# Kernel tuning notes

Hardware: AMD Instinct MI355X
Metric: run time of the kernel (lower is better)

Reference implementation:

```python
import jax, jax.numpy as jnp
import numpy as np
from jax import lax

B, N, R, L = 16, 256, 24, 32
MEAN_STOP_TIME_S = 60.0
AVG_TRANSFER_WAIT_TIME_S = 300.0
SYMMETRIC_ROUTES = True
INF = jnp.inf


def setup_inputs() -> dict:
    key = jax.random.key(0)
    k1, k2, k3 = jax.random.split(key, 3)
    drive_times = jax.random.uniform(k1, (B, N, N), jnp.float32) * 1000.0 + 30.0
    demand = jax.random.uniform(k2, (B, N, N), jnp.float32) * 10.0
    demand = demand * (1.0 - jnp.eye(N, dtype=jnp.float32))  # no self-demand
    batch_routes = jax.random.randint(k3, (B, R, L), 0, N, dtype=jnp.int32)
    return {"drive_times": drive_times, "demand": demand, "batch_routes": batch_routes}


def _route_edges_and_legs(routes, dtm):
    # routes: [B,R,L] node ids (no -1 padding in this setup); dtm: [B,N,N]
    b = jnp.arange(B)[:, None, None]
    sf, st = routes[:, :, :-1], routes[:, :, 1:]
    leg_fwd = dtm[b, sf, st] + MEAN_STOP_TIME_S            # [B,R,L-1]
    zero = jnp.zeros((B, R, 1), dtm.dtype)
    cum_f = jnp.concatenate([zero, jnp.cumsum(leg_fwd, -1)], -1)  # [B,R,L]
    tri = jnp.triu(jnp.ones((L, L), dtype=bool), 1)
    # ride time from stop position i to position j>i along the route
    t_f = jnp.where(tri, cum_f[:, :, None, :] - cum_f[:, :, :, None], INF)
    b4 = jnp.arange(B)[:, None, None, None]
    src = jnp.broadcast_to(routes[:, :, :, None], (B, R, L, L))
    dst = jnp.broadcast_to(routes[:, :, None, :], (B, R, L, L))
    edge = jnp.full((B, N, N), INF, dtm.dtype)
    edge = edge.at[b4, src, dst].min(t_f)
    leg_rev = None
    if SYMMETRIC_ROUTES:
        leg_rev = dtm[b, st, sf] + MEAN_STOP_TIME_S        # reverse-direction legs
        cum_r = jnp.concatenate([zero, jnp.cumsum(leg_rev, -1)], -1)
        t_r = jnp.where(tri, cum_r[:, :, None, :] - cum_r[:, :, :, None], INF)
        edge = edge.at[b4, dst, src].min(t_r)              # ride from s_j back to s_i
    return edge, leg_fwd, leg_rev


def _floyd_warshall(edge):
    # batched FW, also tracking hop count of shortest paths
    idx = jnp.arange(N)
    dist = edge.at[:, idx, idx].set(0.0)
    offdiag = ~jnp.eye(N, dtype=bool)
    hops = jnp.where(jnp.isfinite(dist) & offdiag, 1.0, 0.0)

    def body(carry, k):
        d, h = carry
        dc = lax.dynamic_slice_in_dim(d, k, 1, axis=2)  # [B,N,1]
        dr = lax.dynamic_slice_in_dim(d, k, 1, axis=1)  # [B,1,N]
        hc = lax.dynamic_slice_in_dim(h, k, 1, axis=2)
        hr = lax.dynamic_slice_in_dim(h, k, 1, axis=1)
        alt = dc + dr
        better = alt < d
        return (jnp.where(better, alt, d), jnp.where(better, hc + hr, h)), None

    (dist, hops), _ = lax.scan(body, (dist, hops), idx)
    return dist, hops


def reference(drive_times, demand, batch_routes):
    edge, leg_fwd, leg_rev = _route_edges_and_legs(batch_routes, drive_times)
    dist, hops = _floyd_warshall(edge)
    nopath = jnp.isinf(dist)
    path_lens = jnp.where(nopath, 0.0, hops + 1.0)  # n nodes on path (diag -> 1)
    transfers = jnp.where(path_lens == 0.0, 0.0, path_lens - 2.0)
    trip_times = jnp.where(nopath, 0.0, dist + transfers * AVG_TRANSFER_WAIT_TIME_S)
    total_demand_time = (demand * trip_times).sum((1, 2))
    total_transfers = (demand * transfers).sum((1, 2))
    unserved_demand = jnp.where(nopath, demand, 0.0).sum((1, 2))
    total_demand = demand.sum((1, 2))
    n_disconnected = (nopath & (demand > 0)).sum((1, 2))
    buckets = [jnp.where(transfers == float(ii), demand, 0.0).sum((1, 2)) for ii in range(3)]
    d_un = jnp.where(transfers > 2.0, demand, 0.0).sum((1, 2)) + unserved_demand
    trips_at_transfers = jnp.stack(buckets + [d_un], axis=1)  # [B,4]
    total_route_time = leg_fwd.sum((1, 2))
    if SYMMETRIC_ROUTES:
        total_route_time = total_route_time + leg_rev.sum((1, 2))
    return (total_demand_time, total_route_time, trips_at_transfers,
            total_demand, unserved_demand, total_transfers, trip_times,
            n_disconnected)
```

## Files before the change

### kernel.cpp

```cpp
#include <hip/hip_runtime.h>

#define BB 16
#define NL 256
#define RR 24
#define LL 32
#define NN (NL*NL)
#define BNN (BB*NN)
#define TT 64

#define O_TDT 0
#define O_RT  16
#define O_TAT 32
#define O_TD  96
#define O_UNS 112
#define O_TTR 128
#define O_TT  144
#define O_ND  1048720

#define HSC 9.3132257461547852e-10
#define H2  1073741824.0
#define HMASK 8191

#define RIDX(r, c2) (((r)<<6) + ((((c2) ^ ((r)&31)))<<1))
#define LDD(A, r, c2) (*(double2*)&A[RIDX((r),(c2))])

__global__ __launch_bounds__(1024) void k_init(double2* __restrict__ dist2, float* __restrict__ acc){
    int idx = blockIdx.x*1024 + threadIdx.x;
    double inf = __builtin_huge_val();
    double2 v = make_double2(inf, inf);
    int q = (idx*2) & (NN-1);
    int r = q % 257;
    if (r == 0)   v.x = 0.0;
    if (r == 256) v.y = 0.0;
    dist2[idx] = v;
    if (blockIdx.x == 0 && threadIdx.x < 256) acc[threadIdx.x] = 0.f;
}

__global__ void k_routes(const float* __restrict__ dtm, const int* __restrict__ routes,
                         unsigned long long* __restrict__ dist, float* __restrict__ acc){
    int br = blockIdx.x; int b = br / RR, r = br % RR;
    int lane = threadIdx.x;
    __shared__ int   s[LL];
    __shared__ float lf[LL], lr[LL], cf[LL], cr[LL];
    if (lane < LL) s[lane] = routes[(b*RR + r)*LL + lane];
    __syncthreads();
    if (lane < LL-1){
        int a0 = s[lane], a1 = s[lane+1];
        const float* dt = dtm + b*NN;
        lf[lane] = dt[a0*NL + a1] + 60.0f;
        lr[lane] = dt[a1*NL + a0] + 60.0f;
    }
    __syncthreads();
    if (lane == 0){
        float af = 0.f, ar = 0.f;
        cf[0] = 0.f; cr[0] = 0.f;
        for (int l = 0; l < LL-1; l++){
            af += lf[l]; ar += lr[l];
            cf[l+1] = af; cr[l+1] = ar;
        }
        atomicAdd(&acc[b*16 + 1], af + ar);
    }
    __syncthreads();
    for (int p = lane; p < LL*LL; p += 64){
        int i = p >> 5, j = p & 31;
        if (j > i){
            double vf = (double)(cf[j] - cf[i]) + HSC;
            double vr = (double)(cr[j] - cr[i]) + HSC;
            atomicMin(&dist[b*NN + s[i]*NL + s[j]], (unsigned long long)__double_as_longlong(vf));
            atomicMin(&dist[b*NN + s[j]*NL + s[i]], (unsigned long long)__double_as_longlong(vr));
        }
    }
}

__global__ __launch_bounds__(256, 1) void k_fw_round(
        const double* __restrict__ src, double* __restrict__ dst, int kb){
    int b  = blockIdx.y;
    int m  = blockIdx.x;
    int ti = m >> 2, tj = m & 3;
    int t  = threadIdx.x;
    int r0 = (t >> 4) << 2;
    int c2 = (t & 15) << 1;
    int c4 = (t & 15) << 2;
    __shared__ double KD[4096];
    __shared__ double BD[4096];
    const double* Kg = src + b*NN + kb*TT*(NL+1);
    const double* Bg = src + b*NN + kb*TT*NL + tj*TT;
    const double* Cg = src + b*NN + ti*TT*NL + kb*TT;
    const double* Dg = src + b*NN + ti*TT*NL + tj*TT;

    double2 c0[4][2], d0[4][2];
    #pragma unroll
    for (int i = 0; i < 4; i++){
        c0[i][0] = *(const double2*)(Cg + (r0+i)*NL + c4);
        c0[i][1] = *(const double2*)(Cg + (r0+i)*NL + c4 + 2);
        d0[i][0] = *(const double2*)(Dg + (r0+i)*NL + c4);
        d0[i][1] = *(const double2*)(Dg + (r0+i)*NL + c4 + 2);
    }

    #pragma unroll
    for (int u = 0; u < 8; u++){
        int fid = u*256 + t;
        int row = fid >> 5, cc = fid & 31;
        LDD(KD, row, cc) = *(const double2*)(Kg + row*NL + cc*2);
        LDD(BD, row, cc) = *(const double2*)(Bg + row*NL + cc*2);
    }
    __syncthreads();

    for (int skb = 0; skb < 4; skb++){
        int s0 = skb*16, sc2 = skb*8;
        if (t < 64){
            int i = t >> 2, jg = t & 3, rr = s0 + i, cb = sc2 + jg*2;
            double2 m0 = LDD(KD, rr, cb), m1 = LDD(KD, rr, cb+1);
            double md4[4] = {m0.x, m0.y, m1.x, m1.y};
            #pragma unroll
            for (int k = 0; k < 16; k++){
                double rd[4];
                #pragma unroll
                for (int c = 0; c < 4; c++) rd[c] = __shfl(md4[c], (k<<2)|jg);
                double cd = __shfl(md4[k&3], (i<<2)|(k>>2));
                #pragma unroll
                for (int c = 0; c < 4; c++) md4[c] = fmin(md4[c], cd + rd[c]);
            }
            LDD(KD, rr, cb)   = make_double2(md4[0], md4[1]);
            LDD(KD, rr, cb+1) = make_double2(md4[2], md4[3]);
        }
        __syncthreads();
        int rs_r  = s0 + (t >> 4);
        int rs_c2 = (t & 15) << 1;
        int cs_r  = t >> 2;
        int cs_c2 = sc2 + ((t & 3) << 1);
        double rs[4], cs[4], ar[16], ac[16];
        {
            double2 v0 = LDD(KD, rs_r, rs_c2), v1 = LDD(KD, rs_r, rs_c2+1);
            rs[0]=v0.x; rs[1]=v0.y; rs[2]=v1.x; rs[3]=v1.y;
            double2 w0 = LDD(KD, cs_r, cs_c2), w1 = LDD(KD, cs_r, cs_c2+1);
            cs[0]=w0.x; cs[1]=w0.y; cs[2]=w1.x; cs[3]=w1.y;
            #pragma unroll
            for (int c = 0; c < 8; c++){
                double2 av = LDD(KD, rs_r, sc2 + c);
                ar[2*c] = av.x; ar[2*c+1] = av.y;
                double2 aw = LDD(KD, cs_r, sc2 + c);
                ac[2*c] = aw.x; ac[2*c+1] = aw.y;
            }
        }
        #pragma unroll
        for (int k = 0; k < 16; k++){
            double2 b0 = LDD(KD, s0+k, rs_c2), b1 = LDD(KD, s0+k, rs_c2+1);
            rs[0] = fmin(rs[0], ar[k] + b0.x);
            rs[1] = fmin(rs[1], ar[k] + b0.y);
            rs[2] = fmin(rs[2], ar[k] + b1.x);
            rs[3] = fmin(rs[3], ar[k] + b1.y);
            double2 e0 = LDD(KD, s0+k, cs_c2), e1 = LDD(KD, s0+k, cs_c2+1);
            cs[0] = fmin(cs[0], ac[k] + e0.x);
            cs[1] = fmin(cs[1], ac[k] + e0.y);
            cs[2] = fmin(cs[2], ac[k] + e1.x);
            cs[3] = fmin(cs[3], ac[k] + e1.y);
        }
        __syncthreads();
        LDD(KD, rs_r, rs_c2)   = make_double2(rs[0], rs[1]);
        LDD(KD, rs_r, rs_c2+1) = make_double2(rs[2], rs[3]);
        LDD(KD, cs_r, cs_c2)   = make_double2(cs[0], cs[1]);
        LDD(KD, cs_r, cs_c2+1) = make_double2(cs[2], cs[3]);
        __syncthreads();
        double dd[4][4];
        #pragma unroll
        for (int i = 0; i < 4; i++){
            double2 v0 = LDD(KD, r0+i, c2), v1 = LDD(KD, r0+i, c2+1);
            dd[i][0]=v0.x; dd[i][1]=v0.y; dd[i][2]=v1.x; dd[i][3]=v1.y;
        }
        #pragma unroll
        for (int q4 = 0; q4 < 4; q4++){
            int kr = s0 + q4*4;
            double a[4][4], bm[4][4];
            #pragma unroll
            for (int i = 0; i < 4; i++){
                double2 a0 = LDD(KD, r0+i, sc2+q4*2), a1 = LDD(KD, r0+i, sc2+q4*2+1);
                a[i][0]=a0.x; a[i][1]=a0.y; a[i][2]=a1.x; a[i][3]=a1.y;
            }
            #pragma unroll
            for (int q = 0; q < 4; q++){
                double2 b0 = LDD(KD, kr+q, c2), b1 = LDD(KD, kr+q, c2+1);
                bm[q][0]=b0.x; bm[q][1]=b0.y; bm[q][2]=b1.x; bm[q][3]=b1.y;
            }
            #pragma unroll
            for (int q = 0; q < 4; q++)
            #pragma unroll
            for (int i = 0; i < 4; i++)
            #pragma unroll
            for (int j = 0; j < 4; j++)
                dd[i][j] = fmin(dd[i][j], a[i][q] + bm[q][j]);
        }
        __syncthreads();
        #pragma unroll
        for (int i = 0; i < 4; i++){
            LDD(KD, r0+i, c2)   = make_double2(dd[i][0], dd[i][1]);
            LDD(KD, r0+i, c2+1) = make_double2(dd[i][2], dd[i][3]);
        }
        __syncthreads();
    }

    double inf = __builtin_huge_val();
    double md[4][4];
    #pragma unroll
    for (int i = 0; i < 4; i++)
    #pragma unroll
    for (int j = 0; j < 4; j++) md[i][j] = inf;
    #pragma unroll 4
    for (int q4 = 0; q4 < 16; q4++){
        double a[4][4], bm[4][4];
        #pragma unroll
        for (int i = 0; i < 4; i++){
            double2 a0 = LDD(KD, r0+i, q4*2), a1 = LDD(KD, r0+i, q4*2+1);
            a[i][0]=a0.x; a[i][1]=a0.y; a[i][2]=a1.x; a[i][3]=a1.y;
        }
        int kr = q4*4;
        #pragma unroll
        for (int q = 0; q < 4; q++){
            double2 b0 = LDD(BD, kr+q, c2), b1 = LDD(BD, kr+q, c2+1);
            bm[q][0]=b0.x; bm[q][1]=b0.y; bm[q][2]=b1.x; bm[q][3]=b1.y;
        }
        #pragma unroll
        for (int q = 0; q < 4; q++)
        #pragma unroll
        for (int i = 0; i < 4; i++)
        #pragma unroll
        for (int j = 0; j < 4; j++)
            md[i][j] = fmin(md[i][j], a[i][q] + bm[q][j]);
    }
    __syncthreads();
    #pragma unroll
    for (int i = 0; i < 4; i++){
        LDD(BD, r0+i, c2)   = make_double2(md[i][0], md[i][1]);
        LDD(BD, r0+i, c2+1) = make_double2(md[i][2], md[i][3]);
        LDD(KD, r0+i, c2)   = c0[i][0];
        LDD(KD, r0+i, c2+1) = c0[i][1];
    }
    __syncthreads();

    double dd[4][4];
    #pragma unroll
    for (int i = 0; i < 4; i++){
        dd[i][0]=d0[i][0].x; dd[i][1]=d0[i][0].y; dd[i][2]=d0[i][1].x; dd[i][3]=d0[i][1].y;
    }
    #pragma unroll 4
    for (int q4 = 0; q4 < 16; q4++){
        double a[4][4], bm[4][4];
        #pragma unroll
        for (int i = 0; i < 4; i++){
            double2 a0 = LDD(KD, r0+i, q4*2), a1 = LDD(KD, r0+i, q4*2+1);
            a[i][0]=a0.x; a[i][1]=a0.y; a[i][2]=a1.x; a[i][3]=a1.y;
        }
        int kr = q4*4;
        #pragma unroll
        for (int q = 0; q < 4; q++){
            double2 b0 = LDD(BD, kr+q, c2), b1 = LDD(BD, kr+q, c2+1);
            bm[q][0]=b0.x; bm[q][1]=b0.y; bm[q][2]=b1.x; bm[q][3]=b1.y;
        }
        #pragma unroll
        for (int q = 0; q < 4; q++)
        #pragma unroll
        for (int i = 0; i < 4; i++)
        #pragma unroll
        for (int j = 0; j < 4; j++)
            dd[i][j] = fmin(dd[i][j], a[i][q] + bm[q][j]);
    }
    double* Od = dst + b*NN + ti*TT*NL + tj*TT;
    #pragma unroll
    for (int i = 0; i < 4; i++){
        *(double2*)(Od + (r0+i)*NL + c4)     = make_double2(dd[i][0], dd[i][1]);
        *(double2*)(Od + (r0+i)*NL + c4 + 2) = make_double2(dd[i][2], dd[i][3]);
    }
}

__global__ __launch_bounds__(1024) void k_epi(const double2* __restrict__ dist2,
        const float4* __restrict__ demand4, float* __restrict__ out, float* __restrict__ acc){
    int b = blockIdx.y;
    int fid = (b*NN >> 2) + blockIdx.x*1024 + threadIdx.x;
    long long q2 = (long long)fid * 2;
    double2 va = dist2[q2], vb = dist2[q2+1];
    double vs[4] = {va.x, va.y, vb.x, vb.y};
    float4 mv = demand4[fid];
    float ms[4] = {mv.x, mv.y, mv.z, mv.w};
    float s0=0,s1=0,s2=0,s3=0,s4=0,s5=0,s6=0,s7=0,s8=0;
    float tts[4];
    #pragma unroll
    for (int e = 0; e < 4; e++){
        double v = vs[e];
        bool np = !(v < 1e37);
        double vv = np ? 0.0 : v;
        int h = (int)(((long long)(vv * H2)) & (long long)HMASK);
        float d = (float)vv;
        float dm = ms[e];
        float pl = np ? 0.f : (float)(h + 1);
        float tr = (pl == 0.f) ? 0.f : pl - 2.f;
        float tt = np ? 0.f : d + tr*300.f;
        tts[e] = tt;
        s0 += dm*tt;
        s1 += dm*tr;
        s2 += np ? dm : 0.f;
        s3 += dm;
        s4 += (np && dm > 0.f) ? 1.f : 0.f;
        s5 += (tr == 0.f) ? dm : 0.f;
        s6 += (tr == 1.f) ? dm : 0.f;
        s7 += (tr == 2.f) ? dm : 0.f;
        s8 += (tr > 2.f) ? dm : 0.f;
    }
    ((float4*)(out + O_TT))[fid] = make_float4(tts[0],tts[1],tts[2],tts[3]);
    #define RED(x) { x += __shfl_down(x,32); x += __shfl_down(x,16); x += __shfl_down(x,8); \
                     x += __shfl_down(x,4);  x += __shfl_down(x,2);  x += __shfl_down(x,1); }
    RED(s0) RED(s1) RED(s2) RED(s3) RED(s4) RED(s5) RED(s6) RED(s7) RED(s8)
    __shared__ float red[16][9];
    int w = threadIdx.x >> 6;
    if ((threadIdx.x & 63) == 0){
        red[w][0]=s0; red[w][1]=s1; red[w][2]=s2; red[w][3]=s3; red[w][4]=s4;
        red[w][5]=s5; red[w][6]=s6; red[w][7]=s7; red[w][8]=s8;
    }
    __syncthreads();
    if (threadIdx.x < 9){
        float v = 0.f;
        #pragma unroll
        for (int ww = 0; ww < 16; ww++) v += red[ww][threadIdx.x];
        int slot = (threadIdx.x == 0) ? 0 : threadIdx.x + 1;
        atomicAdd(&acc[b*16 + slot], v);
    }
    __syncthreads();
    __shared__ int isLast;
    if (threadIdx.x == 0){
        unsigned prev = atomicAdd((unsigned int*)(acc + 255), 1u);
        isLast = (prev == 255u) ? 1 : 0;
    }
    __syncthreads();
    if (isLast && threadIdx.x < BB){
        int bb = threadIdx.x;
        float a[10];
        #pragma unroll
        for (int s = 0; s < 10; s++) a[s] = atomicAdd(&acc[bb*16 + s], 0.f);
        out[O_TDT + bb] = a[0];
        out[O_RT  + bb] = a[1];
        out[O_TAT + 4*bb + 0] = a[6];
        out[O_TAT + 4*bb + 1] = a[7];
        out[O_TAT + 4*bb + 2] = a[8];
        out[O_TAT + 4*bb + 3] = a[9] + a[3];
        out[O_TD  + bb] = a[4];
        out[O_UNS + bb] = a[3];
        out[O_TTR + bb] = a[2];
        out[O_ND  + bb] = a[5];
    }
}

extern "C" void kernel_launch(void* const* d_in, const int* in_sizes, int n_in,
                              void* d_out, int out_size, void* d_ws, size_t ws_size,
                              hipStream_t stream){
    (void)in_sizes; (void)n_in; (void)out_size; (void)ws_size;
    const float* dtm    = (const float*)d_in[0];
    const float* demand = (const float*)d_in[1];
    const int*   routes = (const int*)d_in[2];
    float* out   = (float*)d_out;
    double* distA = (double*)d_ws;
    double* distB = distA + BNN;
    float*  acc   = (float*)(distB + BNN);

    k_init  <<<512, 1024, 0, stream>>>((double2*)distA, acc);
    k_routes<<<BB*RR,  64, 0, stream>>>(dtm, routes, (unsigned long long*)distA, acc);
    k_fw_round<<<dim3(16,BB), 256, 0, stream>>>(distA, distB, 0);
    k_fw_round<<<dim3(16,BB), 256, 0, stream>>>(distB, distA, 1);
    k_fw_round<<<dim3(16,BB), 256, 0, stream>>>(distA, distB, 2);
    k_fw_round<<<dim3(16,BB), 256, 0, stream>>>(distB, distA, 3);
    k_epi<<<dim3(16,BB), 1024, 0, stream>>>((const double2*)distA,
                                            (const float4*)demand, out, acc);
}
```

Baseline: 256.5 us.

## Fuse init, routes, blocked FW rounds and epilogue into one persistent kernel

Replaces the seven kernel launches with a single persistent kernel of 256 blocks, one per tile per batch, that synchronises the blocks of each batch through per-batch global atomic barriers. Each block keeps its tile in registers across the Floyd-Warshall rounds and writes it back to global memory only when other tiles need it. The epilogue reduction runs directly from registers, so the final distance matrix is never re-read from memory. This removes launch gaps and global round trips, but depends on all 256 blocks being resident at once to avoid a deadlock, and adds spin-wait barrier cost.

```diff
diff --git a/kernel.cpp b/kernel.cpp
--- a/kernel.cpp
+++ b/kernel.cpp
@@ -24,327 +24,359 @@
 #define RIDX(r, c2) (((r)<<6) + ((((c2) ^ ((r)&31)))<<1))
 #define LDD(A, r, c2) (*(double2*)&A[RIDX((r),(c2))])
 
-__global__ __launch_bounds__(1024) void k_init(double2* __restrict__ dist2, float* __restrict__ acc){
-    int idx = blockIdx.x*1024 + threadIdx.x;
-    double inf = __builtin_huge_val();
-    double2 v = make_double2(inf, inf);
-    int q = (idx*2) & (NN-1);
-    int r = q % 257;
-    if (r == 0)   v.x = 0.0;
-    if (r == 256) v.y = 0.0;
-    dist2[idx] = v;
-    if (blockIdx.x == 0 && threadIdx.x < 256) acc[threadIdx.x] = 0.f;
-}
-
-__global__ void k_routes(const float* __restrict__ dtm, const int* __restrict__ routes,
-                         unsigned long long* __restrict__ dist, float* __restrict__ acc){
-    int br = blockIdx.x; int b = br / RR, r = br % RR;
-    int lane = threadIdx.x;
-    __shared__ int   s[LL];
-    __shared__ float lf[LL], lr[LL], cf[LL], cr[LL];
-    if (lane < LL) s[lane] = routes[(b*RR + r)*LL + lane];
+__global__ __launch_bounds__(512) void k_init0(unsigned* __restrict__ ctr){
+    ctr[threadIdx.x] = 0u;
+}
+
+static __device__ __forceinline__ void bbar(unsigned* c, unsigned tgt){
     __syncthreads();
-    if (lane < LL-1){
-        int a0 = s[lane], a1 = s[lane+1];
-        const float* dt = dtm + b*NN;
-        lf[lane] = dt[a0*NL + a1] + 60.0f;
-        lr[lane] = dt[a1*NL + a0] + 60.0f;
+    if (threadIdx.x == 0){
+        __hip_atomic_fetch_add(c, 1u, __ATOMIC_RELEASE, __HIP_MEMORY_SCOPE_AGENT);
+        while (__hip_atomic_load(c, __ATOMIC_ACQUIRE, __HIP_MEMORY_SCOPE_AGENT) < tgt)
+            __builtin_amdgcn_s_sleep(2);
     }
     __syncthreads();
-    if (lane == 0){
-        float af = 0.f, ar = 0.f;
-        cf[0] = 0.f; cr[0] = 0.f;
-        for (int l = 0; l < LL-1; l++){
-            af += lf[l]; ar += lr[l];
-            cf[l+1] = af; cr[l+1] = ar;
-        }
-        atomicAdd(&acc[b*16 + 1], af + ar);
-    }
-    __syncthreads();
-    for (int p = lane; p < LL*LL; p += 64){
-        int i = p >> 5, j = p & 31;
-        if (j > i){
-            double vf = (double)(cf[j] - cf[i]) + HSC;
-            double vr = (double)(cr[j] - cr[i]) + HSC;
-            atomicMin(&dist[b*NN + s[i]*NL + s[j]], (unsigned long long)__double_as_longlong(vf));
-            atomicMin(&dist[b*NN + s[j]*NL + s[i]], (unsigned long long)__double_as_longlong(vr));
-        }
-    }
-}
-
-__global__ __launch_bounds__(256, 1) void k_fw_round(
-        const double* __restrict__ src, double* __restrict__ dst, int kb){
-    int b  = blockIdx.y;
-    int m  = blockIdx.x;
+}
+
+static __device__ __forceinline__ void mulAcc(double dd[4][4], double* A, double* Bm,
+                                              int r0, int cA, int cB){
+    #pragma unroll 4
+    for (int q4 = 0; q4 < 16; q4++){
+        int kr = q4*4, kc = q4*2;
+        double a[4][4], bm[4][4];
+        #pragma unroll
+        for (int i = 0; i < 4; i++){
+            double2 a0 = LDD(A, r0+i, kc), a1 = LDD(A, r0+i, kc+1);
+            a[i][0]=a0.x; a[i][1]=a0.y; a[i][2]=a1.x; a[i][3]=a1.y;
+        }
+        #pragma unroll
+        for (int q = 0; q < 4; q++){
+            double2 b0 = LDD(Bm, kr+q, cA), b1 = LDD(Bm, kr+q, cB);
+            bm[q][0]=b0.x; bm[q][1]=b0.y; bm[q][2]=b1.x; bm[q][3]=b1.y;
+        }
+        #pragma unroll
+        for (int q = 0; q < 4; q++)
+        #pragma unroll
+        for (int i = 0; i < 4; i++)
+        #pragma unroll
+        for (int j = 0; j < 4; j++)
+            dd[i][j] = fmin(dd[i][j], a[i][q] + bm[q][j]);
+    }
+}
+
+static __device__ __forceinline__ void close64(double* SA, int t, int r0, int cA, int cB){
+    for (int skb = 0; skb < 4; skb++){
+        int s0 = skb*16, sc2 = skb*8;
+        if (t < 64){
+            int i = t >> 2, jg = t & 3, rr = s0 + i, cbk = sc2 + jg*2;
+            double2 m0 = LDD(SA, rr, cbk), m1 = LDD(SA, rr, cbk+1);
+            double md4[4] = {m0.x, m0.y, m1.x, m1.y};
+            #pragma unroll
+            for (int k = 0; k < 16; k++){
+                double rd[4];
+                #pragma unroll
+                for (int c = 0; c < 4; c++) rd[c] = __shfl(md4[c], (k<<2)|jg);
+                double cd = __shfl(md4[k&3], (i<<2)|(k>>2));
+                #pragma unroll
+                for (int c = 0; c < 4; c++) md4[c] = fmin(md4[c], cd + rd[c]);
+            }
+            LDD(SA, rr, cbk)   = make_double2(md4[0], md4[1]);
+            LDD(SA, rr, cbk+1) = make_double2(md4[2], md4[3]);
+        }
+        __syncthreads();
+        double sv[2][4], av[2][16];
+        int wr, wcA, wcB;
+        if (t < 128){
+            wr  = s0 + ((t >> 4) << 1);
+            wcA = t & 15; wcB = wcA + 16;
+        } else {
+            int t2 = t - 128;
+            wr  = (t2 >> 2) << 1;
+            wcA = sc2 + (t2 & 3); wcB = wcA + 4;
+        }
+        #pragma unroll
+        for (int i = 0; i < 2; i++){
+            double2 v0 = LDD(SA, wr+i, wcA), v1 = LDD(SA, wr+i, wcB);
+            sv[i][0]=v0.x; sv[i][1]=v0.y; sv[i][2]=v1.x; sv[i][3]=v1.y;
+            #pragma unroll
+            for (int c = 0; c < 8; c++){
+                double2 av2 = LDD(SA, wr+i, sc2 + c);
+                av[i][2*c] = av2.x; av[i][2*c+1] = av2.y;
+            }
+        }
+        #pragma unroll
+        for (int k = 0; k < 16; k++){
+            double2 b0 = LDD(SA, s0+k, wcA), b1 = LDD(SA, s0+k, wcB);
+            #pragma unroll
+            for (int i = 0; i < 2; i++){
+                double ak = av[i][k];
+                sv[i][0] = fmin(sv[i][0], ak + b0.x);
+                sv[i][1] = fmin(sv[i][1], ak + b0.y);
+                sv[i][2] = fmin(sv[i][2], ak + b1.x);
+                sv[i][3] = fmin(sv[i][3], ak + b1.y);
+            }
+        }
+        __syncthreads();
+        #pragma unroll
+        for (int i = 0; i < 2; i++){
+            LDD(SA, wr+i, wcA) = make_double2(sv[i][0], sv[i][1]);
+            LDD(SA, wr+i, wcB) = make_double2(sv[i][2], sv[i][3]);
+        }
+        __syncthreads();
+        double e[4][4];
+        #pragma unroll
+        for (int i = 0; i < 4; i++){
+            double2 v0 = LDD(SA, r0+i, cA), v1 = LDD(SA, r0+i, cB);
+            e[i][0]=v0.x; e[i][1]=v0.y; e[i][2]=v1.x; e[i][3]=v1.y;
+        }
+        #pragma unroll
+        for (int q4 = 0; q4 < 4; q4++){
+            int kr = s0 + q4*4, kc = sc2 + q4*2;
+            double a[4][4], bm[4][4];
+            #pragma unroll
+            for (int i = 0; i < 4; i++){
+                double2 a0 = LDD(SA, r0+i, kc), a1 = LDD(SA, r0+i, kc+1);
+                a[i][0]=a0.x; a[i][1]=a0.y; a[i][2]=a1.x; a[i][3]=a1.y;
+            }
+            #pragma unroll
+            for (int q = 0; q < 4; q++){
+                double2 b0 = LDD(SA, kr+q, cA), b1 = LDD(SA, kr+q, cB);
+                bm[q][0]=b0.x; bm[q][1]=b0.y; bm[q][2]=b1.x; bm[q][3]=b1.y;
+            }
+            #pragma unroll
+            for (int q = 0; q < 4; q++)
+            #pragma unroll
+            for (int i = 0; i < 4; i++)
+            #pragma unroll
+            for (int j = 0; j < 4; j++)
+                e[i][j] = fmin(e[i][j], a[i][q] + bm[q][j]);
+        }
+        __syncthreads();
+        #pragma unroll
+        for (int i = 0; i < 4; i++){
+            LDD(SA, r0+i, cA) = make_double2(e[i][0], e[i][1]);
+            LDD(SA, r0+i, cB) = make_double2(e[i][2], e[i][3]);
+        }
+        __syncthreads();
+    }
+}
+
+__global__ __launch_bounds__(256, 1) void k_mega(
+        const float* __restrict__ dtm, const int* __restrict__ routes,
+        const float* __restrict__ demand, double* __restrict__ D,
+        float* __restrict__ out, float* __restrict__ acc, unsigned* __restrict__ ctr){
+    int blk = blockIdx.x;
+    int b = blk >> 4, m = blk & 15;
     int ti = m >> 2, tj = m & 3;
     int t  = threadIdx.x;
     int r0 = (t >> 4) << 2;
-    int c2 = (t & 15) << 1;
-    int c4 = (t & 15) << 2;
-    __shared__ double KD[4096];
-    __shared__ double BD[4096];
-    const double* Kg = src + b*NN + kb*TT*(NL+1);
-    const double* Bg = src + b*NN + kb*TT*NL + tj*TT;
-    const double* Cg = src + b*NN + ti*TT*NL + kb*TT;
-    const double* Dg = src + b*NN + ti*TT*NL + tj*TT;
-
-    double2 c0[4][2], d0[4][2];
+    int cA = t & 15, cB = cA + 16;
+    unsigned* cbp = ctr + b*32;
+    double* Tg = D + b*NN + (ti*NL + tj)*TT;
+    __shared__ __align__(16) double SA[4096], SB[4096];
+
+    double inf = __builtin_huge_val();
     #pragma unroll
     for (int i = 0; i < 4; i++){
-        c0[i][0] = *(const double2*)(Cg + (r0+i)*NL + c4);
-        c0[i][1] = *(const double2*)(Cg + (r0+i)*NL + c4 + 2);
-        d0[i][0] = *(const double2*)(Dg + (r0+i)*NL + c4);
-        d0[i][1] = *(const double2*)(Dg + (r0+i)*NL + c4 + 2);
-    }
-
-    #pragma unroll
-    for (int u = 0; u < 8; u++){
-        int fid = u*256 + t;
-        int row = fid >> 5, cc = fid & 31;
-        LDD(KD, row, cc) = *(const double2*)(Kg + row*NL + cc*2);
-        LDD(BD, row, cc) = *(const double2*)(Bg + row*NL + cc*2);
-    }
-    __syncthreads();
-
-    for (int skb = 0; skb < 4; skb++){
-        int s0 = skb*16, sc2 = skb*8;
-        if (t < 64){
-            int i = t >> 2, jg = t & 3, rr = s0 + i, cb = sc2 + jg*2;
-            double2 m0 = LDD(KD, rr, cb), m1 = LDD(KD, rr, cb+1);
-            double md4[4] = {m0.x, m0.y, m1.x, m1.y};
-            #pragma unroll
-            for (int k = 0; k < 16; k++){
-                double rd[4];
-                #pragma unroll
-                for (int c = 0; c < 4; c++) rd[c] = __shfl(md4[c], (k<<2)|jg);
-                double cd = __shfl(md4[k&3], (i<<2)|(k>>2));
-                #pragma unroll
-                for (int c = 0; c < 4; c++) md4[c] = fmin(md4[c], cd + rd[c]);
-            }
-            LDD(KD, rr, cb)   = make_double2(md4[0], md4[1]);
-            LDD(KD, rr, cb+1) = make_double2(md4[2], md4[3]);
-        }
-        __syncthreads();
-        int rs_r  = s0 + (t >> 4);
-        int rs_c2 = (t & 15) << 1;
-        int cs_r  = t >> 2;
-        int cs_c2 = sc2 + ((t & 3) << 1);
-        double rs[4], cs[4], ar[16], ac[16];
-        {
-            double2 v0 = LDD(KD, rs_r, rs_c2), v1 = LDD(KD, rs_r, rs_c2+1);
-            rs[0]=v0.x; rs[1]=v0.y; rs[2]=v1.x; rs[3]=v1.y;
-            double2 w0 = LDD(KD, cs_r, cs_c2), w1 = LDD(KD, cs_r, cs_c2+1);
-            cs[0]=w0.x; cs[1]=w0.y; cs[2]=w1.x; cs[3]=w1.y;
-            #pragma unroll
-            for (int c = 0; c < 8; c++){
-                double2 av = LDD(KD, rs_r, sc2 + c);
-                ar[2*c] = av.x; ar[2*c+1] = av.y;
-                double2 aw = LDD(KD, cs_r, sc2 + c);
-                ac[2*c] = aw.x; ac[2*c+1] = aw.y;
-            }
-        }
-        #pragma unroll
-        for (int k = 0; k < 16; k++){
-            double2 b0 = LDD(KD, s0+k, rs_c2), b1 = LDD(KD, s0+k, rs_c2+1);
-            rs[0] = fmin(rs[0], ar[k] + b0.x);
-            rs[1] = fmin(rs[1], ar[k] + b0.y);
-            rs[2] = fmin(rs[2], ar[k] + b1.x);
-            rs[3] = fmin(rs[3], ar[k] + b1.y);
-            double2 e0 = LDD(KD, s0+k, cs_c2), e1 = LDD(KD, s0+k, cs_c2+1);
-            cs[0] = fmin(cs[0], ac[k] + e0.x);
-            cs[1] = fmin(cs[1], ac[k] + e0.y);
-            cs[2] = fmin(cs[2], ac[k] + e1.x);
-            cs[3] = fmin(cs[3], ac[k] + e1.y);
-        }
-        __syncthreads();
-        LDD(KD, rs_r, rs_c2)   = make_double2(rs[0], rs[1]);
-        LDD(KD, rs_r, rs_c2+1) = make_double2(rs[2], rs[3]);
-        LDD(KD, cs_r, cs_c2)   = make_double2(cs[0], cs[1]);
-        LDD(KD, cs_r, cs_c2+1) = make_double2(cs[2], cs[3]);
-        __syncthreads();
-        double dd[4][4];
-        #pragma unroll
-        for (int i = 0; i < 4; i++){
-            double2 v0 = LDD(KD, r0+i, c2), v1 = LDD(KD, r0+i, c2+1);
-            dd[i][0]=v0.x; dd[i][1]=v0.y; dd[i][2]=v1.x; dd[i][3]=v1.y;
-        }
-        #pragma unroll
-        for (int q4 = 0; q4 < 4; q4++){
-            int kr = s0 + q4*4;
-            double a[4][4], bm[4][4];
+        double2 z0 = make_double2(inf, inf), z1 = z0;
+        if (ti == tj){
+            int gr = r0 + i;
+            if (gr == 2*cA)   z0.x = 0.0;
+            if (gr == 2*cA+1) z0.y = 0.0;
+            if (gr == 2*cB)   z1.x = 0.0;
+            if (gr == 2*cB+1) z1.y = 0.0;
+        }
+        *(double2*)(Tg + (r0+i)*NL + 2*cA) = z0;
+        *(double2*)(Tg + (r0+i)*NL + 2*cB) = z1;
+    }
+    if (m == 0 && t < 16) acc[b*16 + t] = 0.f;
+    bbar(cbp, 16u*1);
+
+    {
+        int w = t >> 6, lane = t & 63;
+        int r = (w == 0) ? m : ((w == 1 && m < 8) ? 16 + m : -1);
+        char* rbase = (char*)SA + w*1024;
+        int*   sS = (int*)rbase;
+        float* lf = (float*)(rbase + 128);
+        float* lr = (float*)(rbase + 256);
+        float* cf = (float*)(rbase + 384);
+        float* cr = (float*)(rbase + 512);
+        if (r >= 0 && lane < LL) sS[lane] = routes[(b*RR + r)*LL + lane];
+        __syncthreads();
+        if (r >= 0 && lane < LL-1){
+            int a0 = sS[lane], a1 = sS[lane+1];
+            const float* dt = dtm + b*NN;
+            lf[lane] = dt[a0*NL + a1] + 60.0f;
+            lr[lane] = dt[a1*NL + a0] + 60.0f;
+        }
+        __syncthreads();
+        if (r >= 0 && lane == 0){
+            float af = 0.f, ar2 = 0.f;
+            cf[0] = 0.f; cr[0] = 0.f;
+            for (int l = 0; l < LL-1; l++){
+                af += lf[l]; ar2 += lr[l];
+                cf[l+1] = af; cr[l+1] = ar2;
+            }
+            atomicAdd(&acc[b*16 + 1], af + ar2);
+        }
+        __syncthreads();
+        if (r >= 0){
+            unsigned long long* db = (unsigned long long*)(D + b*NN);
+            for (int p = lane; p < LL*LL; p += 64){
+                int i = p >> 5, j = p & 31;
+                if (j > i){
+                    double vf = (double)(cf[j] - cf[i]) + HSC;
+                    double vr = (double)(cr[j] - cr[i]) + HSC;
+                    atomicMin(&db[sS[i]*NL + sS[j]], (unsigned long long)__double_as_longlong(vf));
+                    atomicMin(&db[sS[j]*NL + sS[i]], (unsigned long long)__double_as_longlong(vr));
+                }
+            }
+        }
+    }
+    bbar(cbp, 16u*2);
+
+    double dd[4][4];
+    #pragma unroll
+    for (int i = 0; i < 4; i++){
+        double2 v0 = *(const double2*)(Tg + (r0+i)*NL + 2*cA);
+        double2 v1 = *(const double2*)(Tg + (r0+i)*NL + 2*cB);
+        dd[i][0]=v0.x; dd[i][1]=v0.y; dd[i][2]=v1.x; dd[i][3]=v1.y;
+    }
+
+    for (int kb = 0; kb < 4; kb++){
+        bool isDiag = (ti == kb) & (tj == kb);
+        bool isRow  = (ti == kb) && !isDiag;
+        bool isCol  = (tj == kb) && !isDiag;
+        bool inDP   = isDiag | isRow | isCol;
+        if (inDP){
+            if (isDiag){
+                #pragma unroll
+                for (int i = 0; i < 4; i++){
+                    LDD(SA, r0+i, cA) = make_double2(dd[i][0], dd[i][1]);
+                    LDD(SA, r0+i, cB) = make_double2(dd[i][2], dd[i][3]);
+                }
+            } else {
+                #pragma unroll
+                for (int i = 0; i < 4; i++){
+                    LDD(SB, r0+i, cA) = make_double2(dd[i][0], dd[i][1]);
+                    LDD(SB, r0+i, cB) = make_double2(dd[i][2], dd[i][3]);
+                }
+                const double* Kg = D + b*NN + kb*TT*(NL+1);
+                #pragma unroll
+                for (int u = 0; u < 8; u++){
+                    int fid = u*256 + t, row = fid >> 5, cc = fid & 31;
+                    LDD(SA, row, cc) = *(const double2*)(Kg + row*NL + cc*2);
+                }
+            }
+            __syncthreads();
+            close64(SA, t, r0, cA, cB);
+            if (isDiag){
+                #pragma unroll
+                for (int i = 0; i < 4; i++){
+                    double2 v0 = LDD(SA, r0+i, cA), v1 = LDD(SA, r0+i, cB);
+                    dd[i][0]=v0.x; dd[i][1]=v0.y; dd[i][2]=v1.x; dd[i][3]=v1.y;
+                }
+            } else if (isRow){
+                mulAcc(dd, SA, SB, r0, cA, cB);
+            } else {
+                mulAcc(dd, SB, SA, r0, cA, cB);
+            }
             #pragma unroll
             for (int i = 0; i < 4; i++){
-                double2 a0 = LDD(KD, r0+i, sc2+q4*2), a1 = LDD(KD, r0+i, sc2+q4*2+1);
-                a[i][0]=a0.x; a[i][1]=a0.y; a[i][2]=a1.x; a[i][3]=a1.y;
-            }
-            #pragma unroll
-            for (int q = 0; q < 4; q++){
-                double2 b0 = LDD(KD, kr+q, c2), b1 = LDD(KD, kr+q, c2+1);
-                bm[q][0]=b0.x; bm[q][1]=b0.y; bm[q][2]=b1.x; bm[q][3]=b1.y;
-            }
-            #pragma unroll
-            for (int q = 0; q < 4; q++)
-            #pragma unroll
-            for (int i = 0; i < 4; i++)
-            #pragma unroll
-            for (int j = 0; j < 4; j++)
-                dd[i][j] = fmin(dd[i][j], a[i][q] + bm[q][j]);
-        }
-        __syncthreads();
-        #pragma unroll
-        for (int i = 0; i < 4; i++){
-            LDD(KD, r0+i, c2)   = make_double2(dd[i][0], dd[i][1]);
-            LDD(KD, r0+i, c2+1) = make_double2(dd[i][2], dd[i][3]);
-        }
-        __syncthreads();
-    }
-
-    double inf = __builtin_huge_val();
-    double md[4][4];
-    #pragma unroll
-    for (int i = 0; i < 4; i++)
-    #pragma unroll
-    for (int j = 0; j < 4; j++) md[i][j] = inf;
-    #pragma unroll 4
-    for (int q4 = 0; q4 < 16; q4++){
-        double a[4][4], bm[4][4];
-        #pragma unroll
-        for (int i = 0; i < 4; i++){
-            double2 a0 = LDD(KD, r0+i, q4*2), a1 = LDD(KD, r0+i, q4*2+1);
-            a[i][0]=a0.x; a[i][1]=a0.y; a[i][2]=a1.x; a[i][3]=a1.y;
-        }
-        int kr = q4*4;
-        #pragma unroll
-        for (int q = 0; q < 4; q++){
-            double2 b0 = LDD(BD, kr+q, c2), b1 = LDD(BD, kr+q, c2+1);
-            bm[q][0]=b0.x; bm[q][1]=b0.y; bm[q][2]=b1.x; bm[q][3]=b1.y;
-        }
-        #pragma unroll
-        for (int q = 0; q < 4; q++)
-        #pragma unroll
-        for (int i = 0; i < 4; i++)
-        #pragma unroll
-        for (int j = 0; j < 4; j++)
-            md[i][j] = fmin(md[i][j], a[i][q] + bm[q][j]);
-    }
-    __syncthreads();
+                *(double2*)(Tg + (r0+i)*NL + 2*cA) = make_double2(dd[i][0], dd[i][1]);
+                *(double2*)(Tg + (r0+i)*NL + 2*cB) = make_double2(dd[i][2], dd[i][3]);
+            }
+        }
+        bbar(cbp, 16u*(3 + 2*kb));
+        if (!inDP){
+            const double* Xg = D + b*NN + (ti*NL + kb)*TT;
+            const double* Yg = D + b*NN + (kb*NL + tj)*TT;
+            #pragma unroll
+            for (int u = 0; u < 8; u++){
+                int fid = u*256 + t, row = fid >> 5, cc = fid & 31;
+                LDD(SA, row, cc) = *(const double2*)(Xg + row*NL + cc*2);
+                LDD(SB, row, cc) = *(const double2*)(Yg + row*NL + cc*2);
+            }
+            __syncthreads();
+            mulAcc(dd, SA, SB, r0, cA, cB);
+            if (kb != 3){
+                #pragma unroll
+                for (int i = 0; i < 4; i++){
+                    *(double2*)(Tg + (r0+i)*NL + 2*cA) = make_double2(dd[i][0], dd[i][1]);
+                    *(double2*)(Tg + (r0+i)*NL + 2*cB) = make_double2(dd[i][2], dd[i][3]);
+                }
+            }
+        }
+        bbar(cbp, 16u*(4 + 2*kb));
+    }
+
+    float s9[9];
+    #pragma unroll
+    for (int q = 0; q < 9; q++) s9[q] = 0.f;
     #pragma unroll
     for (int i = 0; i < 4; i++){
-        LDD(BD, r0+i, c2)   = make_double2(md[i][0], md[i][1]);
-        LDD(BD, r0+i, c2+1) = make_double2(md[i][2], md[i][3]);
-        LDD(KD, r0+i, c2)   = c0[i][0];
-        LDD(KD, r0+i, c2+1) = c0[i][1];
-    }
-    __syncthreads();
-
-    double dd[4][4];
-    #pragma unroll
-    for (int i = 0; i < 4; i++){
-        dd[i][0]=d0[i][0].x; dd[i][1]=d0[i][0].y; dd[i][2]=d0[i][1].x; dd[i][3]=d0[i][1].y;
-    }
-    #pragma unroll 4
-    for (int q4 = 0; q4 < 16; q4++){
-        double a[4][4], bm[4][4];
-        #pragma unroll
-        for (int i = 0; i < 4; i++){
-            double2 a0 = LDD(KD, r0+i, q4*2), a1 = LDD(KD, r0+i, q4*2+1);
-            a[i][0]=a0.x; a[i][1]=a0.y; a[i][2]=a1.x; a[i][3]=a1.y;
-        }
-        int kr = q4*4;
-        #pragma unroll
-        for (int q = 0; q < 4; q++){
-            double2 b0 = LDD(BD, kr+q, c2), b1 = LDD(BD, kr+q, c2+1);
-            bm[q][0]=b0.x; bm[q][1]=b0.y; bm[q][2]=b1.x; bm[q][3]=b1.y;
-        }
-        #pragma unroll
-        for (int q = 0; q < 4; q++)
-        #pragma unroll
-        for (int i = 0; i < 4; i++)
-        #pragma unroll
-        for (int j = 0; j < 4; j++)
-            dd[i][j] = fmin(dd[i][j], a[i][q] + bm[q][j]);
-    }
-    double* Od = dst + b*NN + ti*TT*NL + tj*TT;
-    #pragma unroll
-    for (int i = 0; i < 4; i++){
-        *(double2*)(Od + (r0+i)*NL + c4)     = make_double2(dd[i][0], dd[i][1]);
-        *(double2*)(Od + (r0+i)*NL + c4 + 2) = make_double2(dd[i][2], dd[i][3]);
-    }
-}
-
-__global__ __launch_bounds__(1024) void k_epi(const double2* __restrict__ dist2,
-        const float4* __restrict__ demand4, float* __restrict__ out, float* __restrict__ acc){
-    int b = blockIdx.y;
-    int fid = (b*NN >> 2) + blockIdx.x*1024 + threadIdx.x;
-    long long q2 = (long long)fid * 2;
-    double2 va = dist2[q2], vb = dist2[q2+1];
-    double vs[4] = {va.x, va.y, vb.x, vb.y};
-    float4 mv = demand4[fid];
-    float ms[4] = {mv.x, mv.y, mv.z, mv.w};
-    float s0=0,s1=0,s2=0,s3=0,s4=0,s5=0,s6=0,s7=0,s8=0;
-    float tts[4];
-    #pragma unroll
-    for (int e = 0; e < 4; e++){
-        double v = vs[e];
-        bool np = !(v < 1e37);
-        double vv = np ? 0.0 : v;
-        int h = (int)(((long long)(vv * H2)) & (long long)HMASK);
-        float d = (float)vv;
-        float dm = ms[e];
-        float pl = np ? 0.f : (float)(h + 1);
-        float tr = (pl == 0.f) ? 0.f : pl - 2.f;
-        float tt = np ? 0.f : d + tr*300.f;
-        tts[e] = tt;
-        s0 += dm*tt;
-        s1 += dm*tr;
-        s2 += np ? dm : 0.f;
-        s3 += dm;
-        s4 += (np && dm > 0.f) ? 1.f : 0.f;
-        s5 += (tr == 0.f) ? dm : 0.f;
-        s6 += (tr == 1.f) ? dm : 0.f;
-        s7 += (tr == 2.f) ? dm : 0.f;
-        s8 += (tr > 2.f) ? dm : 0.f;
-    }
-    ((float4*)(out + O_TT))[fid] = make_float4(tts[0],tts[1],tts[2],tts[3]);
+        const float* dmg = demand + b*NN + (ti*TT + r0 + i)*NL + tj*TT;
+        float* ttg = out + O_TT + b*NN + (ti*TT + r0 + i)*NL + tj*TT;
+        float2 m0 = *(const float2*)(dmg + 2*cA);
+        float2 m1 = *(const float2*)(dmg + 2*cB);
+        float dmv[4] = {m0.x, m0.y, m1.x, m1.y};
+        float tts[4];
+        #pragma unroll
+        for (int e = 0; e < 4; e++){
+            double v = dd[i][e];
+            bool np = !(v < 1e37);
+            double vv = np ? 0.0 : v;
+            int h = (int)(((long long)(vv * H2)) & (long long)HMASK);
+            float d = (float)vv;
+            float dm = dmv[e];
+            float pl = np ? 0.f : (float)(h + 1);
+            float tr = (pl == 0.f) ? 0.f : pl - 2.f;
+            float tt = np ? 0.f : d + tr*300.f;
+            tts[e] = tt;
+            s9[0] += dm*tt;
+            s9[1] += dm*tr;
+            s9[2] += np ? dm : 0.f;
+            s9[3] += dm;
+            s9[4] += (np && dm > 0.f) ? 1.f : 0.f;
+            s9[5] += (tr == 0.f) ? dm : 0.f;
+            s9[6] += (tr == 1.f) ? dm : 0.f;
+            s9[7] += (tr == 2.f) ? dm : 0.f;
+            s9[8] += (tr > 2.f) ? dm : 0.f;
+        }
+        *(float2*)(ttg + 2*cA) = make_float2(tts[0], tts[1]);
+        *(float2*)(ttg + 2*cB) = make_float2(tts[2], tts[3]);
+    }
     #define RED(x) { x += __shfl_down(x,32); x += __shfl_down(x,16); x += __shfl_down(x,8); \
                      x += __shfl_down(x,4);  x += __shfl_down(x,2);  x += __shfl_down(x,1); }
-    RED(s0) RED(s1) RED(s2) RED(s3) RED(s4) RED(s5) RED(s6) RED(s7) RED(s8)
-    __shared__ float red[16][9];
-    int w = threadIdx.x >> 6;
-    if ((threadIdx.x & 63) == 0){
-        red[w][0]=s0; red[w][1]=s1; red[w][2]=s2; red[w][3]=s3; red[w][4]=s4;
-        red[w][5]=s5; red[w][6]=s6; red[w][7]=s7; red[w][8]=s8;
+    #pragma unroll
+    for (int q = 0; q < 9; q++) RED(s9[q])
+    float* red = (float*)SB;
+    int wv = t >> 6;
+    if ((t & 63) == 0){
+        #pragma unroll
+        for (int q = 0; q < 9; q++) red[wv*9 + q] = s9[q];
     }
     __syncthreads();
-    if (threadIdx.x < 9){
-        float v = 0.f;
-        #pragma unroll
-        for (int ww = 0; ww < 16; ww++) v += red[ww][threadIdx.x];
-        int slot = (threadIdx.x == 0) ? 0 : threadIdx.x + 1;
+    if (t < 9){
+        float v = red[t] + red[9+t] + red[18+t] + red[27+t];
+        int slot = (t == 0) ? 0 : t + 1;
         atomicAdd(&acc[b*16 + slot], v);
     }
-    __syncthreads();
-    __shared__ int isLast;
-    if (threadIdx.x == 0){
-        unsigned prev = atomicAdd((unsigned int*)(acc + 255), 1u);
-        isLast = (prev == 255u) ? 1 : 0;
-    }
-    __syncthreads();
-    if (isLast && threadIdx.x < BB){
-        int bb = threadIdx.x;
+    bbar(cbp, 16u*11);
+    if (m == 0 && t == 0){
         float a[10];
         #pragma unroll
-        for (int s = 0; s < 10; s++) a[s] = atomicAdd(&acc[bb*16 + s], 0.f);
-        out[O_TDT + bb] = a[0];
-        out[O_RT  + bb] = a[1];
-        out[O_TAT + 4*bb + 0] = a[6];
-        out[O_TAT + 4*bb + 1] = a[7];
-        out[O_TAT + 4*bb + 2] = a[8];
-        out[O_TAT + 4*bb + 3] = a[9] + a[3];
-        out[O_TD  + bb] = a[4];
-        out[O_UNS + bb] = a[3];
-        out[O_TTR + bb] = a[2];
-        out[O_ND  + bb] = a[5];
+        for (int q = 0; q < 10; q++) a[q] = acc[b*16 + q];
+        out[O_TDT + b] = a[0];
+        out[O_RT  + b] = a[1];
+        out[O_TAT + 4*b + 0] = a[6];
+        out[O_TAT + 4*b + 1] = a[7];
+        out[O_TAT + 4*b + 2] = a[8];
+        out[O_TAT + 4*b + 3] = a[9] + a[3];
+        out[O_TD  + b] = a[4];
+        out[O_UNS + b] = a[3];
+        out[O_TTR + b] = a[2];
+        out[O_ND  + b] = a[5];
     }
 }
 
@@ -355,17 +387,11 @@
     const float* dtm    = (const float*)d_in[0];
     const float* demand = (const float*)d_in[1];
     const int*   routes = (const int*)d_in[2];
-    float* out   = (float*)d_out;
-    double* distA = (double*)d_ws;
-    double* distB = distA + BNN;
-    float*  acc   = (float*)(distB + BNN);
-
-    k_init  <<<512, 1024, 0, stream>>>((double2*)distA, acc);
-    k_routes<<<BB*RR,  64, 0, stream>>>(dtm, routes, (unsigned long long*)distA, acc);
-    k_fw_round<<<dim3(16,BB), 256, 0, stream>>>(distA, distB, 0);
-    k_fw_round<<<dim3(16,BB), 256, 0, stream>>>(distB, distA, 1);
-    k_fw_round<<<dim3(16,BB), 256, 0, stream>>>(distA, distB, 2);
-    k_fw_round<<<dim3(16,BB), 256, 0, stream>>>(distB, distA, 3);
-    k_epi<<<dim3(16,BB), 1024, 0, stream>>>((const double2*)distA,
-                                            (const float4*)demand, out, acc);
-}
+    float* out = (float*)d_out;
+    double*   D   = (double*)d_ws;
+    float*    acc = (float*)(D + BNN);
+    unsigned* ctr = (unsigned*)(acc + 256);
+
+    k_init0<<<1, 512, 0, stream>>>(ctr);
+    k_mega <<<256, 256, 0, stream>>>(dtm, routes, demand, D, out, acc, ctr);
+}
```

Measured after the change: 348.2 us. 35.8% more time.
